# Optimization experiments

Hardware: AMD Instinct MI355X
Metric: run time of the kernel (lower is better)

The kernel has to match this reference:

```python
import jax, jax.numpy as jnp
import numpy as np

N_NODES = 50000

def setup_inputs() -> dict:
    key = jax.random.key(0)
    k1, k2, k3, k4, k5, k6 = jax.random.split(key, 6)
    N, E, D_IN, D_OUT = N_NODES, 800000, 128, 128
    feature = jax.random.normal(k1, (N, D_IN), dtype=jnp.float32)
    src = jax.random.randint(k2, (E,), 0, N, dtype=jnp.int64)
    dst = jax.random.randint(k3, (E,), 0, N, dtype=jnp.int64)
    w = jax.random.uniform(k4, (E,), dtype=jnp.float32)
    W = jax.random.normal(k5, (D_OUT, D_IN), dtype=jnp.float32) * (1.0 / np.sqrt(D_IN))
    b = jax.random.normal(k6, (D_OUT,), dtype=jnp.float32) * 0.01
    return {"feature": feature, "src": src, "dst": dst, "w": w, "W": W, "b": b}

def reference(feature, src, dst, w, W, b):
    # gcn_msg: gather source node features, scale by per-edge weight  [E, D]
    msg = feature[src] * w[:, None]
    # fn.sum: scatter-sum messages into destination nodes  [N, D]
    agg = jax.ops.segment_sum(msg, dst, num_segments=N_NODES)
    # NodeApplyModule: linear + activation
    h = agg @ W.T + b
    return jax.nn.relu(h)
```

## Files before the change

### kernel.cpp

```cpp
#include <hip/hip_runtime.h>

#define D 128
#define TILE_M 64
#define BS_STRIDE 129
#define AS_STRIDE 68
#define WS_STRIDE 136
#define DS_STRIDE 136
#define GEMM_BLOCKS 256
#define BUCKET_BLOCKS 1024
#define CAP 64

typedef __attribute__((ext_vector_type(8))) short short8;
typedef __attribute__((ext_vector_type(4))) float floatx4;
typedef __attribute__((ext_vector_type(4))) unsigned short ushortx4;

__device__ __forceinline__ unsigned short f2bf(float f) {
    unsigned u = __float_as_uint(f);
    u += 0x7fffu + ((u >> 16) & 1u);
    return (unsigned short)(u >> 16);
}

__global__ __launch_bounds__(256) void gemm_bucket(
    const float* __restrict__ feat, const float* __restrict__ Wm,
    unsigned short* __restrict__ tf,
    const int* __restrict__ src, const int* __restrict__ dst,
    const float* __restrict__ w, int* __restrict__ cnt,
    unsigned* __restrict__ ep, int N, int E)
{
    __shared__ unsigned short Ws[128 * WS_STRIDE];
    __shared__ unsigned short Ds[64 * DS_STRIDE];

    if (blockIdx.x >= GEMM_BLOCKS) {
        const int hb = blockIdx.x - GEMM_BLOCKS;
        const int xcd = hb & 7;
        const int blk = hb >> 3;
        const int nblk = BUCKET_BLOCKS >> 3;
        const int lo = (int)((long long)xcd * N / 8);
        const int hi = (int)((long long)(xcd + 1) * N / 8);
        const int E4 = E & ~3;
        for (int e4 = (blk * 256 + threadIdx.x) * 4; e4 < E4; e4 += nblk * 256 * 4) {
            const int4 d4 = *reinterpret_cast<const int4*>(dst + e4);
#pragma unroll
            for (int j = 0; j < 4; ++j) {
                int d = (j == 0) ? d4.x : (j == 1) ? d4.y : (j == 2) ? d4.z : d4.w;
                if (d >= lo && d < hi) {
                    int e = e4 + j;
                    unsigned rec = ((unsigned)f2bf(w[e]) << 16) | (unsigned)src[e];
                    int pos = atomicAdd(&cnt[d], 1);
                    if (pos < CAP)
                        ep[((size_t)d << 6) + pos] = rec;
                }
            }
        }
        if (threadIdx.x == 0 && blk == 0) {
            for (int e = E4; e < E; ++e) {
                int d = dst[e];
                if (d >= lo && d < hi) {
                    unsigned rec = ((unsigned)f2bf(w[e]) << 16) | (unsigned)src[e];
                    int pos = atomicAdd(&cnt[d], 1);
                    if (pos < CAP)
                        ep[((size_t)d << 6) + pos] = rec;
                }
            }
        }
        return;
    }

    const int tid = threadIdx.x;
    for (int idx = tid; idx < 128 * 128 / 4; idx += 256) {
        int r = idx >> 5;
        int c = (idx & 31) * 4;
        const float4 v = reinterpret_cast<const float4*>(Wm)[idx];
        ushortx4 s;
        s[0] = f2bf(v.x); s[1] = f2bf(v.y); s[2] = f2bf(v.z); s[3] = f2bf(v.w);
        *reinterpret_cast<ushortx4*>(&Ws[r * WS_STRIDE + c]) = s;
    }
    __syncthreads();

    const int lane = tid & 63;
    const int wave = tid >> 6;
    const int kq = (lane >> 4) * 8;
    const int ntiles = (N + 63) >> 6;

    for (int t = blockIdx.x; t < ntiles; t += GEMM_BLOCKS) {
        const int node0 = t * 64;
        const int mr = node0 + wave * 16 + (lane & 15);
        const float* arow = feat + (size_t)(mr < N ? mr : (N - 1)) * D + kq;

        short8 a[4];
#pragma unroll
        for (int kt = 0; kt < 4; ++kt) {
            const float* p = arow + kt * 32;
            const float4 lo = *reinterpret_cast<const float4*>(p);
            const float4 hi = *reinterpret_cast<const float4*>(p + 4);
            short8 v;
            v[0] = (short)f2bf(lo.x); v[1] = (short)f2bf(lo.y);
            v[2] = (short)f2bf(lo.z); v[3] = (short)f2bf(lo.w);
            v[4] = (short)f2bf(hi.x); v[5] = (short)f2bf(hi.y);
            v[6] = (short)f2bf(hi.z); v[7] = (short)f2bf(hi.w);
            a[kt] = v;
        }

        floatx4 acc[8];
#pragma unroll
        for (int nt = 0; nt < 8; ++nt) {
            acc[nt][0] = 0.f; acc[nt][1] = 0.f; acc[nt][2] = 0.f; acc[nt][3] = 0.f;
        }
#pragma unroll
        for (int nt = 0; nt < 8; ++nt) {
            const unsigned short* brow = &Ws[(nt * 16 + (lane & 15)) * WS_STRIDE + kq];
#pragma unroll
            for (int kt = 0; kt < 4; ++kt) {
                short8 b = *reinterpret_cast<const short8*>(brow + kt * 32);
                acc[nt] = __builtin_amdgcn_mfma_f32_16x16x32_bf16(a[kt], b, acc[nt], 0, 0, 0);
            }
        }

        __syncthreads();
        const int mlocal = wave * 16 + (lane >> 4) * 4;
        const int col = lane & 15;
#pragma unroll
        for (int r = 0; r < 4; ++r) {
            unsigned short* drow = &Ds[(mlocal + r) * DS_STRIDE + col];
#pragma unroll
            for (int nt = 0; nt < 8; ++nt)
                drow[nt * 16] = f2bf(acc[nt][r]);
        }
        __syncthreads();

        for (int idx = tid; idx < 64 * 16; idx += 256) {
            int row = idx >> 4;
            int chunk = idx & 15;
            int m = node0 + row;
            if (m < N) {
                uint4 v = *reinterpret_cast<const uint4*>(&Ds[row * DS_STRIDE + chunk * 8]);
                *reinterpret_cast<uint4*>(tf + (size_t)m * D + chunk * 8) = v;
            }
        }
    }
}

__global__ __launch_bounds__(256) void csr_gather_bf16(
    const unsigned short* __restrict__ tf, const unsigned* __restrict__ ep,
    const int* __restrict__ cnt, const float* __restrict__ bias,
    float* __restrict__ out, int N)
{
    int node = blockIdx.x * 8 + (threadIdx.x >> 5);
    if (node >= N) return;
    const int lane = threadIdx.x & 31;
    const int c = lane << 2;
    const unsigned* row = ep + ((size_t)node << 6);
    int end = cnt[node];
    end = end < CAP ? end : CAP;
    int i = 0;
    float a0 = 0.f, a1 = 0.f, a2 = 0.f, a3 = 0.f;

#define ACC(Q, W)                                        \
    a0 += __uint_as_float((Q).x << 16) * (W);            \
    a1 += __uint_as_float((Q).x & 0xffff0000u) * (W);    \
    a2 += __uint_as_float((Q).y << 16) * (W);            \
    a3 += __uint_as_float((Q).y & 0xffff0000u) * (W);

    for (; i + 3 < end; i += 4) {
        const uint4 r4 = *reinterpret_cast<const uint4*>(row + i);
        unsigned s0 = r4.x & 0xffffu, s1 = r4.y & 0xffffu;
        unsigned s2 = r4.z & 0xffffu, s3 = r4.w & 0xffffu;
        float w0 = __uint_as_float(r4.x & 0xffff0000u);
        float w1 = __uint_as_float(r4.y & 0xffff0000u);
        float w2 = __uint_as_float(r4.z & 0xffff0000u);
        float w3 = __uint_as_float(r4.w & 0xffff0000u);
        uint2 q0 = *reinterpret_cast<const uint2*>(tf + (size_t)s0 * D + c);
        uint2 q1 = *reinterpret_cast<const uint2*>(tf + (size_t)s1 * D + c);
        uint2 q2 = *reinterpret_cast<const uint2*>(tf + (size_t)s2 * D + c);
        uint2 q3 = *reinterpret_cast<const uint2*>(tf + (size_t)s3 * D + c);
        ACC(q0, w0) ACC(q1, w1) ACC(q2, w2) ACC(q3, w3)
    }
    for (; i < end; ++i) {
        unsigned r = row[i];
        unsigned s0 = r & 0xffffu;
        float w0 = __uint_as_float(r & 0xffff0000u);
        uint2 q0 = *reinterpret_cast<const uint2*>(tf + (size_t)s0 * D + c);
        ACC(q0, w0)
    }
#undef ACC

    const float4 bv = *reinterpret_cast<const float4*>(bias + c);
    float4 r;
    r.x = fmaxf(a0 + bv.x, 0.f);
    r.y = fmaxf(a1 + bv.y, 0.f);
    r.z = fmaxf(a2 + bv.z, 0.f);
    r.w = fmaxf(a3 + bv.w, 0.f);
    *reinterpret_cast<float4*>(out + (size_t)node * D + c) = r;
}

__global__ __launch_bounds__(256) void edge_scatter(
    const float* __restrict__ feat, const int* __restrict__ src,
    const int* __restrict__ dst, const float* __restrict__ w,
    float* __restrict__ agg, int E)
{
    long long idx = (long long)blockIdx.x * 256 + threadIdx.x;
    int e = (int)(idx >> 5);
    if (e >= E) return;
    int c = ((int)idx & 31) << 2;
    int s = src[e];
    int d = dst[e];
    float wv = w[e];
    const float4 f = *reinterpret_cast<const float4*>(feat + (size_t)s * D + c);
    float* a = agg + (size_t)d * D + c;
    atomicAdd(a + 0, f.x * wv);
    atomicAdd(a + 1, f.y * wv);
    atomicAdd(a + 2, f.z * wv);
    atomicAdd(a + 3, f.w * wv);
}

__global__ __launch_bounds__(256) void node_linear(
    const float* __restrict__ in, const float* __restrict__ Wm,
    const float* __restrict__ bias, float* __restrict__ out, int N)
{
    __shared__ float Bs[64 * BS_STRIDE];
    __shared__ float As[TILE_M * AS_STRIDE];
    const int tid = threadIdx.x;
    const int tx = tid & 15;
    const int ty = tid >> 4;
    const int node0 = blockIdx.x * TILE_M;
    float acc[4][8];
#pragma unroll
    for (int i = 0; i < 4; ++i)
#pragma unroll
        for (int jj = 0; jj < 8; ++jj) acc[i][jj] = 0.0f;
    for (int kh = 0; kh < 2; ++kh) {
        const int kbase = kh * 64;
        for (int i = tid; i < 128 * 64; i += 256) {
            int j = i >> 6, k = i & 63;
            Bs[k * BS_STRIDE + j] = Wm[j * 128 + kbase + k];
        }
        for (int i = tid; i < TILE_M * 64; i += 256) {
            int m = i >> 6, k = i & 63;
            int n = node0 + m;
            As[m * AS_STRIDE + k] = (n < N) ? in[(size_t)n * D + kbase + k] : 0.0f;
        }
        __syncthreads();
        for (int k0 = 0; k0 < 64; k0 += 4) {
            float a[4][4];
#pragma unroll
            for (int i = 0; i < 4; ++i) {
                const float4 v = *reinterpret_cast<const float4*>(&As[(ty * 4 + i) * AS_STRIDE + k0]);
                a[i][0] = v.x; a[i][1] = v.y; a[i][2] = v.z; a[i][3] = v.w;
            }
#pragma unroll
            for (int kk = 0; kk < 4; ++kk) {
                float bv[8];
#pragma unroll
                for (int jj = 0; jj < 8; ++jj) bv[jj] = Bs[(k0 + kk) * BS_STRIDE + tx + 16 * jj];
#pragma unroll
                for (int i = 0; i < 4; ++i)
#pragma unroll
                    for (int jj = 0; jj < 8; ++jj) acc[i][jj] += a[i][kk] * bv[jj];
            }
        }
        __syncthreads();
    }
    float bv[8];
#pragma unroll
    for (int jj = 0; jj < 8; ++jj) bv[jj] = bias[tx + 16 * jj];
#pragma unroll
    for (int i = 0; i < 4; ++i) {
        int n = node0 + ty * 4 + i;
        if (n < N) {
            float* o = out + (size_t)n * D;
#pragma unroll
            for (int jj = 0; jj < 8; ++jj) {
                float v = acc[i][jj] + bv[jj];
                o[tx + 16 * jj] = v > 0.0f ? v : 0.0f;
            }
        }
    }
}

extern "C" void kernel_launch(void* const* d_in, const int* in_sizes, int n_in,
                              void* d_out, int out_size, void* d_ws, size_t ws_size,
                              hipStream_t stream) {
    const float* feat = (const float*)d_in[0];
    const int*   src  = (const int*)d_in[1];
    const int*   dst  = (const int*)d_in[2];
    const float* w    = (const float*)d_in[3];
    const float* Wm   = (const float*)d_in[4];
    const float* bias = (const float*)d_in[5];
    float* out = (float*)d_out;

    const int N = in_sizes[0] / D;
    const int E = in_sizes[1];

    const size_t ep_b  = (size_t)N * CAP * 4;
    const size_t cnt_b = (size_t)N * sizeof(int);
    const size_t tf_b  = (size_t)N * D * 2;
    auto align_up = [](size_t x) { return (x + 255) & ~(size_t)255; };

    const size_t need_full = align_up(ep_b) + align_up(cnt_b) + align_up(tf_b);

    if (ws_size >= need_full && N <= 65536 &&
        (long long)E <= (long long)N * (CAP / 4)) {
        char* p = (char*)d_ws;
        unsigned* ep  = (unsigned*)p;  p += align_up(ep_b);
        int*      cnt = (int*)p;       p += align_up(cnt_b);
        unsigned short* tf = (unsigned short*)p;

        (void)hipMemsetAsync(cnt, 0, cnt_b, stream);
        gemm_bucket<<<GEMM_BLOCKS + BUCKET_BLOCKS, 256, 0, stream>>>(
            feat, Wm, tf, src, dst, w, cnt, ep, N, E);
        csr_gather_bf16<<<(N + 7) / 8, 256, 0, stream>>>(tf, ep, cnt, bias, out, N);
    } else {
        (void)hipMemsetAsync(out, 0, (size_t)N * D * sizeof(float), stream);
        long long st = (long long)E * 32;
        edge_scatter<<<(int)((st + 255) / 256), 256, 0, stream>>>(feat, src, dst, w, out, E);
        node_linear<<<(N + TILE_M - 1) / TILE_M, 256, 0, stream>>>(out, Wm, bias, out, N);
    }
}
```

Before: 162.5 us.

## Merge bucketing into GEMM blocks, vectorize edge loads, widen gather per-lane

The fused kernel used to launch separate GEMM blocks and bucketing blocks. Now every one of 768 blocks first does its share of edge bucketing and then its GEMM tiles, which removes the dedicated bucket blocks. The bucketing loop loads src and w as int4/float4 vectors alongside dst instead of doing scalar loads per accepted edge. In the gather kernel each node is handled by 16 lanes reading 8 bf16 values (16 B) each instead of 32 lanes reading 8 B, which halves per-node lane count and widens memory transactions. The trade-offs are that GEMM work now waits behind bucketing inside each block, and the vector loads fetch src and w for edges whose dst falls outside the block's range.

```diff
diff --git a/kernel.cpp b/kernel.cpp
--- a/kernel.cpp
+++ b/kernel.cpp
@@ -6,8 +6,7 @@
 #define AS_STRIDE 68
 #define WS_STRIDE 136
 #define DS_STRIDE 136
-#define GEMM_BLOCKS 256
-#define BUCKET_BLOCKS 1024
+#define GEMM_BLOCKS 768
 #define CAP 64
 
 typedef __attribute__((ext_vector_type(8))) short short8;
@@ -30,22 +29,24 @@
     __shared__ unsigned short Ws[128 * WS_STRIDE];
     __shared__ unsigned short Ds[64 * DS_STRIDE];
 
-    if (blockIdx.x >= GEMM_BLOCKS) {
-        const int hb = blockIdx.x - GEMM_BLOCKS;
-        const int xcd = hb & 7;
-        const int blk = hb >> 3;
-        const int nblk = BUCKET_BLOCKS >> 3;
+    {
+        const int xcd = blockIdx.x & 7;
+        const int blk = blockIdx.x >> 3;
+        const int nblk = GEMM_BLOCKS >> 3;
         const int lo = (int)((long long)xcd * N / 8);
         const int hi = (int)((long long)(xcd + 1) * N / 8);
         const int E4 = E & ~3;
         for (int e4 = (blk * 256 + threadIdx.x) * 4; e4 < E4; e4 += nblk * 256 * 4) {
-            const int4 d4 = *reinterpret_cast<const int4*>(dst + e4);
+            const int4   d4 = *reinterpret_cast<const int4*>(dst + e4);
+            const int4   s4 = *reinterpret_cast<const int4*>(src + e4);
+            const float4 w4 = *reinterpret_cast<const float4*>(w + e4);
 #pragma unroll
             for (int j = 0; j < 4; ++j) {
-                int d = (j == 0) ? d4.x : (j == 1) ? d4.y : (j == 2) ? d4.z : d4.w;
+                int   d  = (j == 0) ? d4.x : (j == 1) ? d4.y : (j == 2) ? d4.z : d4.w;
                 if (d >= lo && d < hi) {
-                    int e = e4 + j;
-                    unsigned rec = ((unsigned)f2bf(w[e]) << 16) | (unsigned)src[e];
+                    int   sj = (j == 0) ? s4.x : (j == 1) ? s4.y : (j == 2) ? s4.z : s4.w;
+                    float wj = (j == 0) ? w4.x : (j == 1) ? w4.y : (j == 2) ? w4.z : w4.w;
+                    unsigned rec = ((unsigned)f2bf(wj) << 16) | (unsigned)sj;
                     int pos = atomicAdd(&cnt[d], 1);
                     if (pos < CAP)
                         ep[((size_t)d << 6) + pos] = rec;
@@ -63,7 +64,6 @@
                 }
             }
         }
-        return;
     }
 
     const int tid = threadIdx.x;
@@ -145,21 +145,26 @@
     const int* __restrict__ cnt, const float* __restrict__ bias,
     float* __restrict__ out, int N)
 {
-    int node = blockIdx.x * 8 + (threadIdx.x >> 5);
+    int node = blockIdx.x * 16 + (threadIdx.x >> 4);
     if (node >= N) return;
-    const int lane = threadIdx.x & 31;
-    const int c = lane << 2;
+    const int lane = threadIdx.x & 15;
+    const int c = lane << 3;
     const unsigned* row = ep + ((size_t)node << 6);
     int end = cnt[node];
     end = end < CAP ? end : CAP;
     int i = 0;
     float a0 = 0.f, a1 = 0.f, a2 = 0.f, a3 = 0.f;
-
-#define ACC(Q, W)                                        \
+    float a4 = 0.f, a5 = 0.f, a6 = 0.f, a7 = 0.f;
+
+#define ACC8(Q, W)                                       \
     a0 += __uint_as_float((Q).x << 16) * (W);            \
     a1 += __uint_as_float((Q).x & 0xffff0000u) * (W);    \
     a2 += __uint_as_float((Q).y << 16) * (W);            \
-    a3 += __uint_as_float((Q).y & 0xffff0000u) * (W);
+    a3 += __uint_as_float((Q).y & 0xffff0000u) * (W);    \
+    a4 += __uint_as_float((Q).z << 16) * (W);            \
+    a5 += __uint_as_float((Q).z & 0xffff0000u) * (W);    \
+    a6 += __uint_as_float((Q).w << 16) * (W);            \
+    a7 += __uint_as_float((Q).w & 0xffff0000u) * (W);
 
     for (; i + 3 < end; i += 4) {
         const uint4 r4 = *reinterpret_cast<const uint4*>(row + i);
@@ -169,28 +174,35 @@
         float w1 = __uint_as_float(r4.y & 0xffff0000u);
         float w2 = __uint_as_float(r4.z & 0xffff0000u);
         float w3 = __uint_as_float(r4.w & 0xffff0000u);
-        uint2 q0 = *reinterpret_cast<const uint2*>(tf + (size_t)s0 * D + c);
-        uint2 q1 = *reinterpret_cast<const uint2*>(tf + (size_t)s1 * D + c);
-        uint2 q2 = *reinterpret_cast<const uint2*>(tf + (size_t)s2 * D + c);
-        uint2 q3 = *reinterpret_cast<const uint2*>(tf + (size_t)s3 * D + c);
-        ACC(q0, w0) ACC(q1, w1) ACC(q2, w2) ACC(q3, w3)
+        uint4 q0 = *reinterpret_cast<const uint4*>(tf + (size_t)s0 * D + c);
+        uint4 q1 = *reinterpret_cast<const uint4*>(tf + (size_t)s1 * D + c);
+        uint4 q2 = *reinterpret_cast<const uint4*>(tf + (size_t)s2 * D + c);
+        uint4 q3 = *reinterpret_cast<const uint4*>(tf + (size_t)s3 * D + c);
+        ACC8(q0, w0) ACC8(q1, w1) ACC8(q2, w2) ACC8(q3, w3)
     }
     for (; i < end; ++i) {
         unsigned r = row[i];
         unsigned s0 = r & 0xffffu;
         float w0 = __uint_as_float(r & 0xffff0000u);
-        uint2 q0 = *reinterpret_cast<const uint2*>(tf + (size_t)s0 * D + c);
-        ACC(q0, w0)
-    }
-#undef ACC
-
-    const float4 bv = *reinterpret_cast<const float4*>(bias + c);
-    float4 r;
-    r.x = fmaxf(a0 + bv.x, 0.f);
-    r.y = fmaxf(a1 + bv.y, 0.f);
-    r.z = fmaxf(a2 + bv.z, 0.f);
-    r.w = fmaxf(a3 + bv.w, 0.f);
-    *reinterpret_cast<float4*>(out + (size_t)node * D + c) = r;
+        uint4 q0 = *reinterpret_cast<const uint4*>(tf + (size_t)s0 * D + c);
+        ACC8(q0, w0)
+    }
+#undef ACC8
+
+    const float4 bv0 = *reinterpret_cast<const float4*>(bias + c);
+    const float4 bv1 = *reinterpret_cast<const float4*>(bias + c + 4);
+    float4 r0, r1;
+    r0.x = fmaxf(a0 + bv0.x, 0.f);
+    r0.y = fmaxf(a1 + bv0.y, 0.f);
+    r0.z = fmaxf(a2 + bv0.z, 0.f);
+    r0.w = fmaxf(a3 + bv0.w, 0.f);
+    r1.x = fmaxf(a4 + bv1.x, 0.f);
+    r1.y = fmaxf(a5 + bv1.y, 0.f);
+    r1.z = fmaxf(a6 + bv1.z, 0.f);
+    r1.w = fmaxf(a7 + bv1.w, 0.f);
+    float* o = out + (size_t)node * D + c;
+    *reinterpret_cast<float4*>(o) = r0;
+    *reinterpret_cast<float4*>(o + 4) = r1;
 }
 
 __global__ __launch_bounds__(256) void edge_scatter(
@@ -306,9 +318,9 @@
         unsigned short* tf = (unsigned short*)p;
 
         (void)hipMemsetAsync(cnt, 0, cnt_b, stream);
-        gemm_bucket<<<GEMM_BLOCKS + BUCKET_BLOCKS, 256, 0, stream>>>(
+        gemm_bucket<<<GEMM_BLOCKS, 256, 0, stream>>>(
             feat, Wm, tf, src, dst, w, cnt, ep, N, E);
-        csr_gather_bf16<<<(N + 7) / 8, 256, 0, stream>>>(tf, ep, cnt, bias, out, N);
+        csr_gather_bf16<<<(N + 15) / 16, 256, 0, stream>>>(tf, ep, cnt, bias, out, N);
     } else {
         (void)hipMemsetAsync(out, 0, (size_t)N * D * sizeof(float), stream);
         long long st = (long long)E * 32;
```

New measurement: 162.0 us. No clear change (-0.3%).
